# Kernel tuning notes

Measured on AMD Instinct MI355X. Metric: run time of the kernel, lower is better.

The kernel has to match this reference:

```python
import jax, jax.numpy as jnp
import numpy as np
import math

VOCAB = 50000
EMB_DIM = 300
D_MODEL = 2048
BATCH = 4
SEQ = 8192


def setup_inputs() -> dict:
    key = jax.random.key(0)
    k1, k2, k3, k4 = jax.random.split(key, 4)
    x = jax.random.randint(k1, (BATCH, SEQ), 0, VOCAB, dtype=jnp.int64 if jax.config.jax_enable_x64 else jnp.int32)
    emb = jax.random.normal(k2, (VOCAB, EMB_DIM), dtype=jnp.float32)
    # nn.Linear(300, d_model): weight [d_model, 300] in torch; store transposed [300, d_model]
    W = jax.random.normal(k3, (EMB_DIM, D_MODEL), dtype=jnp.float32) * (1.0 / math.sqrt(EMB_DIM))
    b = jax.random.normal(k4, (D_MODEL,), dtype=jnp.float32) * 0.01
    return {"x": x, "emb": emb, "W": W, "b": b}


def reference(x, emb, W, b):
    # Dict lookup per token == single gather: [B, S] -> [B, S, 300]
    vecs = emb[x]
    # Linear(300 -> d_model) then scale by sqrt(d_model)
    out = jnp.einsum("bse,ed->bsd", vecs, W) + b
    return out * jnp.sqrt(jnp.asarray(W.shape[1], dtype=out.dtype))
```

## Files before the change

kernel.cpp:

```cpp
#include <hip/hip_runtime.h>
#include <hip/hip_bf16.h>


#define TOKENS 32768
#define EMB 300
#define DM 2048
#define KPAD 320
#define LDS_STRIDE 72
#define SCALE 45.25483399593904f

typedef _Float16 f16;
typedef _Float16 h4 __attribute__((ext_vector_type(4)));
typedef _Float16 h8 __attribute__((ext_vector_type(8)));
typedef float f32x4 __attribute__((ext_vector_type(4)));

__global__ __launch_bounds__(256) void prep_w(const float* __restrict__ W, f16* __restrict__ Wt) {
    int idx = blockIdx.x * 256 + threadIdx.x;
    int k = idx >> 11;
    int n = idx & 2047;
    f16 v = (f16)0.f;
    if (k < EMB) v = (f16)W[k * DM + n];
    Wt[(size_t)n * KPAD + k] = v;
}

__global__ __launch_bounds__(256) void prep_b(const float* __restrict__ b, float* __restrict__ bs) {
    int i = blockIdx.x * 256 + threadIdx.x;
    if (i < DM) bs[i] = b[i] * SCALE;
}

__global__ __launch_bounds__(256) void embed_gemm(
        const int* __restrict__ x, const float* __restrict__ emb,
        const f16* __restrict__ Wt, const float* __restrict__ bs,
        float* __restrict__ out)
{
    __shared__ __align__(16) f16 As[128 * LDS_STRIDE];
    __shared__ __align__(16) f16 Bs[128 * LDS_STRIDE];
    __shared__ int toks[128];

    const int t = threadIdx.x;
    const int lane = t & 63;
    const int wave = t >> 6;
    const int m0 = blockIdx.y << 7;
    const int n0 = blockIdx.x << 7;
    const int wm = (wave >> 1) << 6;
    const int wn = (wave & 1) << 6;
    const int quad = lane >> 4;
    const int lr = lane & 15;

    if (t < 128) toks[t] = x[m0 + t];
    __syncthreads();

    f32x4 acc[4][4] = {};

    for (int kc = 0; kc < 5; ++kc) {
        const int k0 = kc << 6;

        #pragma unroll
        for (int i = 0; i < 8; ++i) {
            int q   = (i << 8) + t;
            int row = q >> 4;
            int qc  = q & 15;
            h4 v = *(const h4*)(Wt + (size_t)(n0 + row) * KPAD + k0 + (qc << 2));
            *(h4*)(Bs + row * LDS_STRIDE + (qc << 2)) = v;
        }

        #pragma unroll
        for (int i = 0; i < 8; ++i) {
            int q   = (i << 8) + t;
            int row = q >> 4;
            int qc  = q & 15;
            int k   = k0 + (qc << 2);
            h4 hv = {(f16)0.f, (f16)0.f, (f16)0.f, (f16)0.f};
            if (k + 3 < EMB) {
                float4 v = *(const float4*)(emb + (size_t)toks[row] * EMB + k);
                hv[0] = (f16)v.x; hv[1] = (f16)v.y; hv[2] = (f16)v.z; hv[3] = (f16)v.w;
            }
            *(h4*)(As + row * LDS_STRIDE + (qc << 2)) = hv;
        }
        __syncthreads();

        #pragma unroll
        for (int kk = 0; kk < 2; ++kk) {
            h8 af[4], bfr[4];
            const int c = (kk << 2) + quad;
            #pragma unroll
            for (int mi = 0; mi < 4; ++mi) {
                int m = wm + (mi << 4) + lr;
                af[mi] = *(const h8*)(As + m * LDS_STRIDE + (c << 3));
            }
            #pragma unroll
            for (int ni = 0; ni < 4; ++ni) {
                int n = wn + (ni << 4) + lr;
                bfr[ni] = *(const h8*)(Bs + n * LDS_STRIDE + (c << 3));
            }
            #pragma unroll
            for (int mi = 0; mi < 4; ++mi)
                #pragma unroll
                for (int ni = 0; ni < 4; ++ni)
                    acc[mi][ni] = __builtin_amdgcn_mfma_f32_16x16x32_f16(
                        af[mi], bfr[ni], acc[mi][ni], 0, 0, 0);
        }
        __syncthreads();
    }

    #pragma unroll
    for (int ni = 0; ni < 4; ++ni) {
        int n = n0 + wn + (ni << 4) + lr;
        float bias = bs[n];
        #pragma unroll
        for (int mi = 0; mi < 4; ++mi) {
            int mb = m0 + wm + (mi << 4) + (quad << 2);
            #pragma unroll
            for (int r = 0; r < 4; ++r) {
                out[(size_t)(mb + r) * DM + n] = fmaf(acc[mi][ni][r], SCALE, bias);
            }
        }
    }
}

__global__ __launch_bounds__(256) void naive_kernel(
        const int* __restrict__ x, const float* __restrict__ emb,
        const float* __restrict__ W, const float* __restrict__ b, float* __restrict__ out)
{
    size_t idx = (size_t)blockIdx.x * 256 + threadIdx.x;
    int n = (int)(idx & (DM - 1));
    size_t m = idx >> 11;
    const float* e = emb + (size_t)x[m] * EMB;
    float a = 0.f;
    for (int k = 0; k < EMB; ++k) a = fmaf(e[k], W[(size_t)k * DM + n], a);
    out[idx] = (a + b[n]) * SCALE;
}

extern "C" void kernel_launch(void* const* d_in, const int* in_sizes, int n_in,
                              void* d_out, int out_size, void* d_ws, size_t ws_size,
                              hipStream_t stream) {
    const int*   x   = (const int*)d_in[0];
    const float* emb = (const float*)d_in[1];
    const float* W   = (const float*)d_in[2];
    const float* b   = (const float*)d_in[3];
    float* out = (float*)d_out;

    const size_t wt_bytes = (size_t)DM * KPAD * sizeof(f16);
    const size_t need = wt_bytes + (size_t)DM * sizeof(float);

    if (ws_size >= need) {
        f16* Wt = (f16*)d_ws;
        float* bsp = (float*)((char*)d_ws + wt_bytes);
        prep_w<<<(DM * KPAD) / 256, 256, 0, stream>>>(W, Wt);
        prep_b<<<DM / 256, 256, 0, stream>>>(b, bsp);
        dim3 grid(DM / 128, TOKENS / 128);
        embed_gemm<<<grid, 256, 0, stream>>>(x, emb, Wt, bsp, out);
    } else {
        naive_kernel<<<((size_t)TOKENS * DM) / 256, 256, 0, stream>>>(x, emb, W, b, out);
    }
}
```

Baseline: 465.8 us.

## Swizzle LDS tiles, remap blocks per XCD, and tile-transpose weight prep

Replaces the padded LDS layout with an XOR-swizzled 64-wide layout, so B tiles can be loaded with 16-byte vectors and MFMA fragment reads stay free of bank conflicts. It moves to a 1D grid that groups consecutive m-tiles on the same XCD so each XCD's L2 sees the same token rows reused across all n-tiles. The weight transpose prep now goes through an LDS tile with coalesced float4 reads instead of strided scalar writes, and launch bounds request 4 blocks per CU. Risks include mapping assumptions tied to 8 XCDs and extra register pressure from the occupancy hint.

```diff
diff --git a/kernel.cpp b/kernel.cpp
--- a/kernel.cpp
+++ b/kernel.cpp
@@ -6,7 +6,6 @@
 #define EMB 300
 #define DM 2048
 #define KPAD 320
-#define LDS_STRIDE 72
 #define SCALE 45.25483399593904f
 
 typedef _Float16 f16;
@@ -15,12 +14,35 @@
 typedef float f32x4 __attribute__((ext_vector_type(4)));
 
 __global__ __launch_bounds__(256) void prep_w(const float* __restrict__ W, f16* __restrict__ Wt) {
-    int idx = blockIdx.x * 256 + threadIdx.x;
-    int k = idx >> 11;
-    int n = idx & 2047;
-    f16 v = (f16)0.f;
-    if (k < EMB) v = (f16)W[k * DM + n];
-    Wt[(size_t)n * KPAD + k] = v;
+    __shared__ f16 tile[64 * 68];
+    const int k0 = blockIdx.x << 6;
+    const int n0 = blockIdx.y << 6;
+    const int t = threadIdx.x;
+    #pragma unroll
+    for (int i = 0; i < 4; ++i) {
+        int idx = (i << 8) + t;
+        int kr = idx >> 4;
+        int nc = idx & 15;
+        h4 hv = {};
+        if (k0 + kr < EMB) {
+            float4 v = *(const float4*)(W + (size_t)(k0 + kr) * DM + n0 + (nc << 2));
+            hv[0]=(f16)v.x; hv[1]=(f16)v.y; hv[2]=(f16)v.z; hv[3]=(f16)v.w;
+        }
+        *(h4*)(tile + kr * 68 + (nc << 2)) = hv;
+    }
+    __syncthreads();
+    #pragma unroll
+    for (int i = 0; i < 4; ++i) {
+        int idx = (i << 8) + t;
+        int n  = idx >> 4;
+        int kc = idx & 15;
+        h4 hv;
+        hv[0] = tile[(kc * 4 + 0) * 68 + n];
+        hv[1] = tile[(kc * 4 + 1) * 68 + n];
+        hv[2] = tile[(kc * 4 + 2) * 68 + n];
+        hv[3] = tile[(kc * 4 + 3) * 68 + n];
+        *(h4*)(Wt + (size_t)(n0 + n) * KPAD + k0 + (kc << 2)) = hv;
+    }
 }
 
 __global__ __launch_bounds__(256) void prep_b(const float* __restrict__ b, float* __restrict__ bs) {
@@ -28,20 +50,26 @@
     if (i < DM) bs[i] = b[i] * SCALE;
 }
 
-__global__ __launch_bounds__(256) void embed_gemm(
+__global__ __launch_bounds__(256, 4) void embed_gemm(
         const int* __restrict__ x, const float* __restrict__ emb,
         const f16* __restrict__ Wt, const float* __restrict__ bs,
         float* __restrict__ out)
 {
-    __shared__ __align__(16) f16 As[128 * LDS_STRIDE];
-    __shared__ __align__(16) f16 Bs[128 * LDS_STRIDE];
+    __shared__ __align__(16) f16 As[128 * 64];
+    __shared__ __align__(16) f16 Bs[128 * 64];
     __shared__ int toks[128];
+
+    const int lin  = blockIdx.x;
+    const int xcd  = lin & 7;
+    const int slot = lin >> 3;
+    const int mtile = (xcd << 5) + (slot >> 4);
+    const int ntile = slot & 15;
+    const int m0 = mtile << 7;
+    const int n0 = ntile << 7;
 
     const int t = threadIdx.x;
     const int lane = t & 63;
     const int wave = t >> 6;
-    const int m0 = blockIdx.y << 7;
-    const int n0 = blockIdx.x << 7;
     const int wm = (wave >> 1) << 6;
     const int wn = (wave & 1) << 6;
     const int quad = lane >> 4;
@@ -56,12 +84,12 @@
         const int k0 = kc << 6;
 
         #pragma unroll
-        for (int i = 0; i < 8; ++i) {
-            int q   = (i << 8) + t;
-            int row = q >> 4;
-            int qc  = q & 15;
-            h4 v = *(const h4*)(Wt + (size_t)(n0 + row) * KPAD + k0 + (qc << 2));
-            *(h4*)(Bs + row * LDS_STRIDE + (qc << 2)) = v;
+        for (int i = 0; i < 4; ++i) {
+            int idx = (i << 8) + t;
+            int row = idx >> 3;
+            int c   = idx & 7;
+            h8 v = *(const h8*)(Wt + (size_t)(n0 + row) * KPAD + k0 + (c << 3));
+            *(h8*)(Bs + (row << 6) + ((c ^ (row & 7)) << 3)) = v;
         }
 
         #pragma unroll
@@ -70,12 +98,13 @@
             int row = q >> 4;
             int qc  = q & 15;
             int k   = k0 + (qc << 2);
-            h4 hv = {(f16)0.f, (f16)0.f, (f16)0.f, (f16)0.f};
+            h4 hv = {};
             if (k + 3 < EMB) {
                 float4 v = *(const float4*)(emb + (size_t)toks[row] * EMB + k);
-                hv[0] = (f16)v.x; hv[1] = (f16)v.y; hv[2] = (f16)v.z; hv[3] = (f16)v.w;
+                hv[0]=(f16)v.x; hv[1]=(f16)v.y; hv[2]=(f16)v.z; hv[3]=(f16)v.w;
             }
-            *(h4*)(As + row * LDS_STRIDE + (qc << 2)) = hv;
+            int c = qc >> 1, half = qc & 1;
+            *(h4*)(As + (row << 6) + (((c ^ (row & 7)) << 3) + (half << 2))) = hv;
         }
         __syncthreads();
 
@@ -86,12 +115,12 @@
             #pragma unroll
             for (int mi = 0; mi < 4; ++mi) {
                 int m = wm + (mi << 4) + lr;
-                af[mi] = *(const h8*)(As + m * LDS_STRIDE + (c << 3));
+                af[mi] = *(const h8*)(As + (m << 6) + ((c ^ (m & 7)) << 3));
             }
             #pragma unroll
             for (int ni = 0; ni < 4; ++ni) {
                 int n = wn + (ni << 4) + lr;
-                bfr[ni] = *(const h8*)(Bs + n * LDS_STRIDE + (c << 3));
+                bfr[ni] = *(const h8*)(Bs + (n << 6) + ((c ^ (n & 7)) << 3));
             }
             #pragma unroll
             for (int mi = 0; mi < 4; ++mi)
@@ -146,10 +175,9 @@
     if (ws_size >= need) {
         f16* Wt = (f16*)d_ws;
         float* bsp = (float*)((char*)d_ws + wt_bytes);
-        prep_w<<<(DM * KPAD) / 256, 256, 0, stream>>>(W, Wt);
+        prep_w<<<dim3(KPAD / 64, DM / 64), 256, 0, stream>>>(W, Wt);
         prep_b<<<DM / 256, 256, 0, stream>>>(b, bsp);
-        dim3 grid(DM / 128, TOKENS / 128);
-        embed_gemm<<<grid, 256, 0, stream>>>(x, emb, Wt, bsp, out);
+        embed_gemm<<<(TOKENS / 128) * (DM / 128), 256, 0, stream>>>(x, emb, Wt, bsp, out);
     } else {
         naive_kernel<<<((size_t)TOKENS * DM) / 256, 256, 0, stream>>>(x, emb, W, b, out);
     }
```

Measured after the change: 414.4 us. 1.12x faster.
